# Optimization experiments

Measured on AMD Instinct MI355X. Metric: run time of the kernel, lower is better.

## Reference

```python
import jax, jax.numpy as jnp
import numpy as np

INPUTS = 512    # feature dim per timestep == seq len T == max_length (required by module math)
HIDDEN = 512
OUTPUTS = 512
MAXLEN = INPUTS
BATCH = 256


def setup_inputs() -> dict:
    key = jax.random.key(0)
    ks = jax.random.split(key, 7)
    def lin(k, out_f, in_f):
        bound = 1.0 / np.sqrt(in_f)
        return jax.random.uniform(k, (out_f, in_f), jnp.float32, -bound, bound)
    return {
        "x": jax.random.normal(ks[0], (BATCH, INPUTS * MAXLEN), jnp.float32),
        "W_attn": lin(ks[1], MAXLEN, HIDDEN + INPUTS),
        "b_attn": jnp.zeros((MAXLEN,), jnp.float32),
        "W_comb": lin(ks[2], HIDDEN, INPUTS + MAXLEN),
        "b_comb": jnp.zeros((HIDDEN,), jnp.float32),
        "W_ih": lin(ks[3], 3 * HIDDEN, HIDDEN),
        "W_hh": lin(ks[4], 3 * HIDDEN, HIDDEN),
        "b_ih": jnp.zeros((3 * HIDDEN,), jnp.float32),
        "b_hh": jnp.zeros((3 * HIDDEN,), jnp.float32),
        "W_out": lin(ks[5], OUTPUTS, HIDDEN),
        "b_out": jnp.zeros((OUTPUTS,), jnp.float32),
    }


def reference(x, W_attn, b_attn, W_comb, b_comb, W_ih, W_hh, b_ih, b_hh, W_out, b_out):
    B = x.shape[0]
    H = HIDDEN
    xv = x.reshape(B, INPUTS, MAXLEN)      # [B, inputs, T]
    xs = jnp.transpose(xv, (2, 0, 1))      # [T, B, inputs] for scan over time

    def step(h, x_t):
        # Bahdanau-style attention over the inputs axis (M == inputs)
        aw = jax.nn.softmax(jnp.concatenate([x_t, h], axis=1) @ W_attn.T + b_attn, axis=1)  # [B, M]
        ctx = jnp.einsum('bm,bmt->bt', aw, xv)                                              # [B, T]
        g = jax.nn.relu(jnp.concatenate([x_t, ctx], axis=1) @ W_comb.T + b_comb)            # [B, H]
        # PyTorch GRU cell, gate order (r, z, n)
        gi = g @ W_ih.T + b_ih
        gh = h @ W_hh.T + b_hh
        r = jax.nn.sigmoid(gi[:, :H] + gh[:, :H])
        z = jax.nn.sigmoid(gi[:, H:2 * H] + gh[:, H:2 * H])
        n = jnp.tanh(gi[:, 2 * H:] + r * gh[:, 2 * H:])
        h_new = (1.0 - z) * n + z * h
        return h_new, None

    h0 = jnp.zeros((B, H), x.dtype)
    hT, _ = jax.lax.scan(step, h0, xs)
    return hT @ W_out.T + b_out  # [B, outputs]
```

## Files before the change

### kernel.cpp

```cpp
#include <hip/hip_runtime.h>

#define NB 256
#define NT 512
#define NI 512
#define NH 512
#define NG 1536
#define NBLK 512

typedef __attribute__((ext_vector_type(8))) short bf16x8;
typedef __attribute__((ext_vector_type(4))) float f32x4;
typedef __attribute__((ext_vector_type(2))) float f32x2;

#define MFMA(a, b, c) __builtin_amdgcn_mfma_f32_16x16x32_bf16((a), (b), (c), 0, 0, 0)

#define BAR_LEAF(g)   ((g) * 64)
#define BAR_ROOT      1024
#define BAR_GEN       1088
#define FLG_LOGIT(rt) (1152 + (rt) * 64)
#define FLG_GH(rt)    (1664 + (rt) * 64)
#define FLG_XT        1920
#define FLG_G(rg)     (2176 + (rg) * 64)
#define FLG_GP(b)     (2688 + (b) * 64)
#define BAR_WORDS     20480

__device__ __forceinline__ unsigned short f2bf(float f) {
  unsigned int u = __float_as_uint(f);
  u = u + 0x7FFFu + ((u >> 16) & 1u);
  return (unsigned short)(u >> 16);
}
__device__ __forceinline__ float bflo(unsigned int p) { return __uint_as_float(p << 16); }
__device__ __forceinline__ float bfhi(unsigned int p) { return __uint_as_float(p & 0xffff0000u); }
__device__ __forceinline__ float sigm(float x) { return 1.f / (1.f + __expf(-x)); }

__device__ __forceinline__ void stf(float* p, float v) {
  __hip_atomic_store(p, v, __ATOMIC_RELAXED, __HIP_MEMORY_SCOPE_AGENT);
}
__device__ __forceinline__ void stu32(void* p, unsigned v) {
  __hip_atomic_store((unsigned*)p, v, __ATOMIC_RELAXED, __HIP_MEMORY_SCOPE_AGENT);
}
__device__ __forceinline__ void stu64(void* p, unsigned long long v) {
  __hip_atomic_store((unsigned long long*)p, v, __ATOMIC_RELAXED, __HIP_MEMORY_SCOPE_AGENT);
}
__device__ __forceinline__ void ldg16(uint4& d, const void* p) {
  asm volatile("global_load_dwordx4 %0, %1, off sc1" : "=v"(d) : "v"(p));
}
__device__ __forceinline__ void ldg8(float2& d, const void* p) {
  asm volatile("global_load_dwordx2 %0, %1, off sc1" : "=v"(d) : "v"(p));
}
__device__ __forceinline__ void ldg4(float& d, const void* p) {
  asm volatile("global_load_dword %0, %1, off sc1" : "=v"(d) : "v"(p));
}
__device__ __forceinline__ void wait_vm0() {
  asm volatile("s_waitcnt vmcnt(0)" ::: "memory");
  __builtin_amdgcn_sched_barrier(0);
}
__device__ __forceinline__ bf16x8 as_frag(uint4 v) {
  union { uint4 u; bf16x8 f; } c; c.u = v; return c.f;
}

__device__ __forceinline__ void flag_add(unsigned* f) {
  __hip_atomic_fetch_add(f, 1u, __ATOMIC_RELAXED, __HIP_MEMORY_SCOPE_AGENT);
}
__device__ __forceinline__ void flag_wait(unsigned* f, unsigned target) {
  while (__hip_atomic_load(f, __ATOMIC_RELAXED, __HIP_MEMORY_SCOPE_AGENT) < target)
    __builtin_amdgcn_s_sleep(1);
}

#define FP8_FMA16(PX, A_, ACC) do {                                              \
    f32x2 d0 = __builtin_amdgcn_cvt_pk_f32_fp8((int)(PX).x, false);              \
    f32x2 d1 = __builtin_amdgcn_cvt_pk_f32_fp8((int)(PX).x, true);               \
    f32x2 d2 = __builtin_amdgcn_cvt_pk_f32_fp8((int)(PX).y, false);              \
    f32x2 d3 = __builtin_amdgcn_cvt_pk_f32_fp8((int)(PX).y, true);               \
    f32x2 d4 = __builtin_amdgcn_cvt_pk_f32_fp8((int)(PX).z, false);              \
    f32x2 d5 = __builtin_amdgcn_cvt_pk_f32_fp8((int)(PX).z, true);               \
    f32x2 d6 = __builtin_amdgcn_cvt_pk_f32_fp8((int)(PX).w, false);              \
    f32x2 d7 = __builtin_amdgcn_cvt_pk_f32_fp8((int)(PX).w, true);               \
    (ACC)[0]  = fmaf((A_), d0[0], (ACC)[0]);  (ACC)[1]  = fmaf((A_), d0[1], (ACC)[1]);  \
    (ACC)[2]  = fmaf((A_), d1[0], (ACC)[2]);  (ACC)[3]  = fmaf((A_), d1[1], (ACC)[3]);  \
    (ACC)[4]  = fmaf((A_), d2[0], (ACC)[4]);  (ACC)[5]  = fmaf((A_), d2[1], (ACC)[5]);  \
    (ACC)[6]  = fmaf((A_), d3[0], (ACC)[6]);  (ACC)[7]  = fmaf((A_), d3[1], (ACC)[7]);  \
    (ACC)[8]  = fmaf((A_), d4[0], (ACC)[8]);  (ACC)[9]  = fmaf((A_), d4[1], (ACC)[9]);  \
    (ACC)[10] = fmaf((A_), d5[0], (ACC)[10]); (ACC)[11] = fmaf((A_), d5[1], (ACC)[11]); \
    (ACC)[12] = fmaf((A_), d6[0], (ACC)[12]); (ACC)[13] = fmaf((A_), d6[1], (ACC)[13]); \
    (ACC)[14] = fmaf((A_), d7[0], (ACC)[14]); (ACC)[15] = fmaf((A_), d7[1], (ACC)[15]); \
  } while (0)

__global__ __launch_bounds__(256) void cast_f32_bf16(const float* __restrict__ s,
                                                     unsigned short* __restrict__ d, int n) {
  int i = blockIdx.x * 256 + threadIdx.x;
  int stride = gridDim.x * 256;
  for (; i < n; i += stride) d[i] = f2bf(s[i]);
}

__global__ __launch_bounds__(256) void zt_fp8(unsigned short* __restrict__ XZ,
                                              float* __restrict__ Zsc,
                                              const unsigned short* __restrict__ Wc) {
  __shared__ unsigned short As[32][552];
  __shared__ float Zf[32][512];
  const int tid = threadIdx.x;
  const int row0 = blockIdx.x * 32;
  const uint4* src = (const uint4*)(XZ + (size_t)row0 * 512);
#pragma unroll
  for (int it = 0; it < 8; ++it) {
    int e8 = tid + it * 256;
    uint4 v = src[e8];
    *(uint4*)&As[e8 >> 6][(e8 & 63) * 8] = v;
  }
  __syncthreads();
  const int lane = tid & 63, w = tid >> 6;
  const int al = lane & 15, kg = lane >> 4;
  const int rbase = (w & 1) * 16;
  const int cbase = (w >> 1) * 256;
  for (int cc = 0; cc < 16; ++cc) {
    int col0 = cbase + cc * 16;
    f32x4 acc = {0.f, 0.f, 0.f, 0.f};
    const unsigned short* Bp = Wc + (size_t)(col0 + al) * 1024 + 512;
    for (int k = 0; k < 512; k += 32) {
      bf16x8 av = *(const bf16x8*)&As[rbase + al][k + kg * 8];
      bf16x8 bv = *(const bf16x8*)(Bp + k + kg * 8);
      acc = MFMA(av, bv, acc);
    }
#pragma unroll
    for (int r = 0; r < 4; ++r)
      Zf[rbase + kg * 4 + r][col0 + al] = acc[r];
  }
  __syncthreads();
  unsigned char* Z8 = (unsigned char*)XZ + ((size_t)blockIdx.x << 15);
#pragma unroll 2
  for (int r8 = 0; r8 < 8; ++r8) {
    int row = w * 8 + r8;
    const float* vr = &Zf[row][lane * 8];
    float v0 = vr[0], v1 = vr[1], v2 = vr[2], v3 = vr[3];
    float v4 = vr[4], v5 = vr[5], v6 = vr[6], v7 = vr[7];
    float amax = fmaxf(fmaxf(fmaxf(fabsf(v0), fabsf(v1)), fmaxf(fabsf(v2), fabsf(v3))),
                       fmaxf(fmaxf(fabsf(v4), fabsf(v5)), fmaxf(fabsf(v6), fabsf(v7))));
#pragma unroll
    for (int off = 32; off >= 1; off >>= 1) amax = fmaxf(amax, __shfl_xor(amax, off));
    float inv = amax > 0.f ? 448.f / amax : 0.f;
    int w0 = __builtin_amdgcn_cvt_pk_fp8_f32(v0 * inv, v1 * inv, 0, false);
    w0 = __builtin_amdgcn_cvt_pk_fp8_f32(v2 * inv, v3 * inv, w0, true);
    int w1 = __builtin_amdgcn_cvt_pk_fp8_f32(v4 * inv, v5 * inv, 0, false);
    w1 = __builtin_amdgcn_cvt_pk_fp8_f32(v6 * inv, v7 * inv, w1, true);
    uint2 o; o.x = (unsigned)w0; o.y = (unsigned)w1;
    *(uint2*)(Z8 + ((size_t)row << 9) + lane * 8) = o;
    if (lane == 0) Zsc[row0 + row] = amax * (1.f / 448.f);
  }
}

__global__ __launch_bounds__(256) void init_kernel(const float* __restrict__ x,
                                                   unsigned short* __restrict__ Xt,
                                                   unsigned short* __restrict__ Hbf,
                                                   unsigned* __restrict__ bar) {
  int idx = blockIdx.x * 256 + threadIdx.x;
  if (idx < BAR_WORDS) bar[idx] = 0u;
  if (idx < NB * NI) {
    int b = idx >> 9, i = idx & 511;
    Xt[idx] = f2bf(x[((size_t)b * 512 + i) * 512]);
    Hbf[idx] = 0;
  }
}

__global__ __launch_bounds__(256) void lxgx0_kernel(const unsigned short* __restrict__ Xt0,
                                                    const unsigned short* __restrict__ Wa,
                                                    const unsigned short* __restrict__ Wc,
                                                    const float* __restrict__ b_comb,
                                                    float* __restrict__ Lx,
                                                    float* __restrict__ Gx) {
  const int tid = threadIdx.x, lane = tid & 63, w = tid >> 6;
  const int al = lane & 15, kg = lane >> 4;
  int T = blockIdx.x;
  int m = T >> 7, tt = T & 127;
  int rt = tt >> 4, ct = tt & 15;
  int row0 = rt * 32 + (w & 1) * 16, col0 = ct * 32 + (w >> 1) * 16;
  const unsigned short* A = Xt0 + (size_t)(row0 + al) * NI;
  const unsigned short* B = (m ? Wc : Wa) + (size_t)(col0 + al) * 1024;
  f32x4 acc = {0.f, 0.f, 0.f, 0.f};
  for (int k = 0; k < 512; k += 32)
    acc = MFMA(*(const bf16x8*)(A + k + kg * 8), *(const bf16x8*)(B + k + kg * 8), acc);
  float* dst = m ? Gx : Lx;
  float bias = m ? b_comb[col0 + al] : 0.f;
#pragma unroll
  for (int r = 0; r < 4; ++r) {
    int row = row0 + kg * 4 + r;
    dst[row * NI + col0 + al] = acc[r] + bias;
  }
}

struct KParams {
  const unsigned char* Z8;
  const float* Zsc;
  const unsigned short* Wa;
  const unsigned short* Whh;
  const unsigned short* Wc;
  const unsigned short* Wih;
  const unsigned short* Wout;
  unsigned short* Xt;
  unsigned short* Hbf;
  unsigned short* Gbf;
  float* logits;
  float* gh;
  float* Lx;
  float* Gx;
  float* Gp;
  const float* x;
  const float* b_attn;
  const float* b_hh;
  const float* b_ih;
  const float* b_comb;
  const float* b_out;
  float* out;
  unsigned* bar;
};

__device__ __forceinline__ void gbar(unsigned* bar, unsigned gen_expect) {
  asm volatile("s_waitcnt vmcnt(0)" ::: "memory");
  __syncthreads();
  if (threadIdx.x == 0) {
    unsigned old = __hip_atomic_fetch_add(&bar[BAR_LEAF(blockIdx.x >> 5)], 1u,
                                          __ATOMIC_RELAXED, __HIP_MEMORY_SCOPE_AGENT);
    if ((old & 31) == 31) {
      unsigned ro = __hip_atomic_fetch_add(&bar[BAR_ROOT], 1u,
                                           __ATOMIC_RELAXED, __HIP_MEMORY_SCOPE_AGENT);
      if ((ro & 15) == 15)
        __hip_atomic_fetch_add(&bar[BAR_GEN], 1u,
                               __ATOMIC_RELAXED, __HIP_MEMORY_SCOPE_AGENT);
    }
    while (__hip_atomic_load(&bar[BAR_GEN], __ATOMIC_RELAXED, __HIP_MEMORY_SCOPE_AGENT) < gen_expect)
      __builtin_amdgcn_s_sleep(2);
    asm volatile("" ::: "memory");
  }
  __syncthreads();
}

__global__ __launch_bounds__(256, 2) void persistent_kernel(KParams P) {
  __shared__ __align__(16) unsigned char Zlds[65536];
  __shared__ float aw[512];
  __shared__ float pS[4][32][16];
  __shared__ float red[8];
  const int bid = blockIdx.x, tid = threadIdx.x;
  const int lane = tid & 63, w = tid >> 6;
  const int al = lane & 15, kg = lane >> 4;

  f32x4 hreg = {0.f, 0.f, 0.f, 0.f};

  const int b2_ = bid >> 1, mh_ = bid & 1;
  {
    const unsigned char* src = P.Z8 + ((size_t)(b2_ * 16 + mh_ * 8 + w * 2) << 15)
                               + (size_t)lane * 16;
    unsigned char* dst = &Zlds[w * 16384 + lane * 16];
#pragma unroll
    for (int k = 0; k < 16; ++k) {
      uint4 v = *(const uint4*)(src + ((size_t)k << 10));
      *(uint4*)(dst + (k << 10)) = v;
    }
  }

  for (int t = 0; t < NT; ++t) {
    const int p = t & 1, np = p ^ 1;
    if (bid < 128) {
      int rt = bid >> 4, ct = bid & 15;
      int row0 = rt * 32 + (w & 1) * 16, col0 = ct * 32 + (w >> 1) * 16;
      const unsigned short* Ah = P.Hbf + (size_t)(row0 + al) * NH;
      const unsigned short* B = P.Wa + (size_t)(col0 + al) * 1024 + 512;
      uint4 fh[16];
      float lx[4];
#pragma unroll
      for (int i = 0; i < 16; ++i) ldg16(fh[i], Ah + i * 32 + kg * 8);
      {
        const float* lxp = P.Lx + (size_t)p * (NB * NI) + (size_t)(row0 + kg * 4) * NI + col0 + al;
#pragma unroll
        for (int r = 0; r < 4; ++r) ldg4(lx[r], lxp + (size_t)r * NI);
      }
      wait_vm0();
      f32x4 a1 = {0.f, 0.f, 0.f, 0.f};
#pragma unroll
      for (int i = 0; i < 16; ++i)
        a1 = MFMA(as_frag(fh[i]), *(const bf16x8*)(B + i * 32 + kg * 8), a1);
#pragma unroll
      for (int r = 0; r < 4; ++r) {
        int row = row0 + kg * 4 + r;
        stf(&P.logits[row * NI + col0 + al], lx[r] + a1[r] + P.b_attn[col0 + al]);
      }
      __syncthreads();
      if (tid == 0) flag_add(&P.bar[FLG_LOGIT(rt)]);
    } else if (bid < 320) {
      int bb = bid - 128;
      int rt = bb / 48, ct = bb % 48;
      int row0 = rt * 64 + w * 16, col0 = ct * 32;
      const unsigned short* Ah = P.Hbf + (size_t)(row0 + al) * NH;
      const unsigned short* B0 = P.Whh + (size_t)(col0 + al) * 512;
      const unsigned short* B1 = P.Whh + (size_t)(col0 + 16 + al) * 512;
      uint4 fa[16];
#pragma unroll
      for (int i = 0; i < 16; ++i) ldg16(fa[i], Ah + i * 32 + kg * 8);
      wait_vm0();
      f32x4 a0 = {0.f, 0.f, 0.f, 0.f}, a1 = {0.f, 0.f, 0.f, 0.f};
#pragma unroll
      for (int i = 0; i < 16; ++i) {
        a0 = MFMA(as_frag(fa[i]), *(const bf16x8*)(B0 + i * 32 + kg * 8), a0);
        a1 = MFMA(as_frag(fa[i]), *(const bf16x8*)(B1 + i * 32 + kg * 8), a1);
      }
#pragma unroll
      for (int r = 0; r < 4; ++r) {
        int row = row0 + kg * 4 + r;
        stf(&P.gh[row * NG + col0 + al], a0[r] + P.b_hh[col0 + al]);
        stf(&P.gh[row * NG + col0 + 16 + al], a1[r] + P.b_hh[col0 + 16 + al]);
      }
      __syncthreads();
      if (tid == 0) flag_add(&P.bar[FLG_GH(rt)]);
    } else if (bid < 384) {
    } else {
      if (t < NT - 1) {
        for (int e2 = (bid - 384) * 256 + tid; e2 < NB * NI / 2; e2 += 128 * 256) {
          int b = e2 >> 8, i = (e2 & 255) * 2;
          const float* xp = P.x + ((size_t)b * 512 + i) * 512 + t + 1;
          unsigned lo = f2bf(xp[0]);
          unsigned hi = f2bf(xp[512]);
          stu32(&P.Xt[(size_t)np * (NB * NI) + b * 512 + i], lo | (hi << 16));
        }
        __syncthreads();
        if (tid == 0) flag_add(&P.bar[FLG_XT]);
      }
    }

    {
      const int b = b2_, mh = mh_;
      if (tid == 0) flag_wait(&P.bar[FLG_LOGIT(b >> 5)], 16u * (t + 1));
      __syncthreads();
      float2 lv;
      ldg8(lv, P.logits + (size_t)b * NI + 2 * tid);
      wait_vm0();
      float mx = fmaxf(lv.x, lv.y);
#pragma unroll
      for (int off = 32; off >= 1; off >>= 1) mx = fmaxf(mx, __shfl_xor(mx, off));
      if (lane == 0) red[w] = mx;
      __syncthreads();
      mx = fmaxf(fmaxf(red[0], red[1]), fmaxf(red[2], red[3]));
      float e0 = __expf(lv.x - mx), e1 = __expf(lv.y - mx);
      float sm = e0 + e1;
#pragma unroll
      for (int off = 32; off >= 1; off >>= 1) sm += __shfl_xor(sm, off);
      if (lane == 0) red[4 + w] = sm;
      __syncthreads();
      sm = (red[4] + red[5]) + (red[6] + red[7]);
      float inv = 1.f / sm;
      float2 scl = *(const float2*)(P.Zsc + (size_t)b * 512 + 2 * tid);
      aw[2 * tid] = e0 * inv * scl.x;
      aw[2 * tid + 1] = e1 * inv * scl.y;
      __syncthreads();

      const int half = lane >> 5, hl = lane & 31;
      const unsigned char* Zb1 = P.Z8 + ((size_t)(b * 16 + mh * 8 + w * 2 + 1) << 15)
                                + (size_t)lane * 16;
      const float* awp = aw + mh * 256 + w * 64;
      float acc[16];
#pragma unroll
      for (int i = 0; i < 16; ++i) acc[i] = 0.f;
      uint4 px[16];
#pragma unroll
      for (int k = 0; k < 16; ++k) px[k] = *(const uint4*)(Zb1 + ((size_t)k << 10));
      const unsigned char* Zl = &Zlds[w * 16384 + lane * 16];
#pragma unroll
      for (int k = 0; k < 16; ++k) {
        uint4 pl = *(const uint4*)(Zl + (k << 10));
        float a_ = awp[2 * k + half];
        FP8_FMA16(pl, a_, acc);
      }
#pragma unroll
      for (int k = 0; k < 16; ++k) {
        float a_ = awp[32 + 2 * k + half];
        FP8_FMA16(px[k], a_, acc);
      }
#pragma unroll
      for (int i = 0; i < 16; ++i) acc[i] += __shfl_xor(acc[i], 32);
      if (lane < 32) {
#pragma unroll
        for (int i = 0; i < 16; ++i) pS[w][hl][i] = acc[i];
      }
      __syncthreads();
      const int c0 = 2 * tid, c1 = 2 * tid + 1;
      float s0 = (pS[0][c0 >> 4][c0 & 15] + pS[1][c0 >> 4][c0 & 15])
               + (pS[2][c0 >> 4][c0 & 15] + pS[3][c0 >> 4][c0 & 15]);
      float s1 = (pS[0][c1 >> 4][c1 & 15] + pS[1][c1 >> 4][c1 & 15])
               + (pS[2][c1 >> 4][c1 & 15] + pS[3][c1 >> 4][c1 & 15]);
      if (mh == 0) {
        union { float f[2]; unsigned long long q; } q0;
        q0.f[0] = s0; q0.f[1] = s1;
        stu64(&P.Gp[(size_t)b * NH + c0], q0.q);
        __syncthreads();
        if (tid == 0) flag_add(&P.bar[FLG_GP(b)]);
      } else {
        __syncthreads();
        if (tid == 0) flag_wait(&P.bar[FLG_GP(b)], (unsigned)(t + 1));
        __syncthreads();
        float2 gp2, gx2;
        ldg8(gp2, &P.Gp[(size_t)b * NH + c0]);
        ldg8(gx2, P.Gx + (size_t)p * (NB * NH) + (size_t)b * NH + c0);
        wait_vm0();
        float v0 = fmaxf(gx2.x + gp2.x + s0, 0.f);
        float v1 = fmaxf(gx2.y + gp2.y + s1, 0.f);
        stu32(&P.Gbf[(size_t)b * NH + c0], (unsigned)f2bf(v0) | ((unsigned)f2bf(v1) << 16));
        __syncthreads();
        if (tid == 0) flag_add(&P.bar[FLG_G(b >> 5)]);
      }
    }

    if (bid >= 384) {
      int q = bid - 384;
      int rt = q >> 4, ct = q & 15;
      int row0 = rt * 32 + (w & 1) * 16;
      int j0 = ct * 32 + (w >> 1) * 16;
      if (tid == 0) {
        flag_wait(&P.bar[FLG_G(rt)], 32u * (t + 1));
        flag_wait(&P.bar[FLG_GH(rt >> 1)], 48u * (t + 1));
      }
      __syncthreads();
      const unsigned short* Ag = P.Gbf + (size_t)(row0 + al) * NH;
      const unsigned short* Br = P.Wih + (size_t)(j0 + al) * 512;
      const unsigned short* Bz = P.Wih + (size_t)(j0 + 512 + al) * 512;
      const unsigned short* Bn = P.Wih + (size_t)(j0 + 1024 + al) * 512;
      int j = j0 + al;
      uint4 fa[16];
      float ghv[4][3];
#pragma unroll
      for (int i = 0; i < 16; ++i) ldg16(fa[i], Ag + i * 32 + kg * 8);
#pragma unroll
      for (int r = 0; r < 4; ++r) {
        const float* ghrow = P.gh + (size_t)(row0 + kg * 4 + r) * NG + j;
        ldg4(ghv[r][0], ghrow);
        ldg4(ghv[r][1], ghrow + 512);
        ldg4(ghv[r][2], ghrow + 1024);
      }
      wait_vm0();
      f32x4 ar = {0.f, 0.f, 0.f, 0.f}, az = {0.f, 0.f, 0.f, 0.f}, an = {0.f, 0.f, 0.f, 0.f};
#pragma unroll
      for (int i = 0; i < 16; ++i) {
        ar = MFMA(as_frag(fa[i]), *(const bf16x8*)(Br + i * 32 + kg * 8), ar);
        az = MFMA(as_frag(fa[i]), *(const bf16x8*)(Bz + i * 32 + kg * 8), az);
        an = MFMA(as_frag(fa[i]), *(const bf16x8*)(Bn + i * 32 + kg * 8), an);
      }
      float bir = P.b_ih[j], biz = P.b_ih[j + 512], bin_ = P.b_ih[j + 1024];
#pragma unroll
      for (int r = 0; r < 4; ++r) {
        int row = row0 + kg * 4 + r;
        float rg = sigm(ar[r] + bir + ghv[r][0]);
        float zg = sigm(az[r] + biz + ghv[r][1]);
        float ng = tanhf(an[r] + bin_ + rg * ghv[r][2]);
        float hn = (1.f - zg) * ng + zg * hreg[r];
        hreg[r] = hn;
        unsigned hv = f2bf(hn);
        unsigned ov = __shfl_xor((int)hv, 1);
        if ((al & 1) == 0)
          stu32(&P.Hbf[(size_t)row * NH + (j & ~1)], hv | (ov << 16));
      }
    } else if (bid >= 320) {
      if (t < NT - 1) {
        if (tid == 0) flag_wait(&P.bar[FLG_XT], 128u * (t + 1));
        __syncthreads();
        int q = bid - 320;
        for (int jj = 0; jj < 4; ++jj) {
          int T = q + 64 * jj;
          int m = T >> 7, tt = T & 127;
          int rt = tt >> 4, ct = tt & 15;
          int row0 = rt * 32 + (w & 1) * 16, col0 = ct * 32 + (w >> 1) * 16;
          const unsigned short* A = P.Xt + (size_t)np * (NB * NI) + (size_t)(row0 + al) * NI;
          const unsigned short* B = (m ? P.Wc : P.Wa) + (size_t)(col0 + al) * 1024;
          uint4 fa[16];
#pragma unroll
          for (int i = 0; i < 16; ++i) ldg16(fa[i], A + i * 32 + kg * 8);
          wait_vm0();
          f32x4 acc = {0.f, 0.f, 0.f, 0.f};
#pragma unroll
          for (int i = 0; i < 16; ++i)
            acc = MFMA(as_frag(fa[i]), *(const bf16x8*)(B + i * 32 + kg * 8), acc);
          float* dst = (m ? P.Gx : P.Lx) + (size_t)np * (NB * NI);
          float bias = m ? P.b_comb[col0 + al] : 0.f;
#pragma unroll
          for (int r = 0; r < 4; ++r) {
            int row = row0 + kg * 4 + r;
            stf(&dst[row * NI + col0 + al], acc[r] + bias);
          }
        }
      }
    }
    gbar(P.bar, (unsigned)(t + 1));
  }

  if (bid < 128) {
    int rt = bid >> 4, ct = bid & 15;
    int row0 = rt * 32 + (w & 1) * 16;
    int col0 = ct * 32 + (w >> 1) * 16;
    const unsigned short* Ah = P.Hbf + (size_t)(row0 + al) * NH;
    const unsigned short* B0 = P.Wout + (size_t)(col0 + al) * 512;
    uint4 fa[16];
#pragma unroll
    for (int i = 0; i < 16; ++i) ldg16(fa[i], Ah + i * 32 + kg * 8);
    wait_vm0();
    f32x4 acc = {0.f, 0.f, 0.f, 0.f};
#pragma unroll
    for (int i = 0; i < 16; ++i) acc = MFMA(as_frag(fa[i]), *(const bf16x8*)(B0 + i * 32 + kg * 8), acc);
#pragma unroll
    for (int r = 0; r < 4; ++r) {
      int row = row0 + kg * 4 + r;
      P.out[row * 512 + col0 + al] = acc[r] + P.b_out[col0 + al];
    }
  }
}

extern "C" void kernel_launch(void* const* d_in, const int* in_sizes, int n_in,
                              void* d_out, int out_size, void* d_ws, size_t ws_size,
                              hipStream_t stream) {
  const float* x      = (const float*)d_in[0];
  const float* W_attn = (const float*)d_in[1];
  const float* b_attn = (const float*)d_in[2];
  const float* W_comb = (const float*)d_in[3];
  const float* b_comb = (const float*)d_in[4];
  const float* W_ih   = (const float*)d_in[5];
  const float* W_hh   = (const float*)d_in[6];
  const float* b_ih   = (const float*)d_in[7];
  const float* b_hh   = (const float*)d_in[8];
  const float* W_out  = (const float*)d_in[9];
  const float* b_out  = (const float*)d_in[10];

  char* wp = (char*)d_ws;
  size_t off = 0;
  unsigned short* XZ   = (unsigned short*)(wp + off); off += (size_t)NB * NI * NH * 2;
  unsigned short* Wa   = (unsigned short*)(wp + off); off += (size_t)NI * 1024 * 2;
  unsigned short* Whh  = (unsigned short*)(wp + off); off += (size_t)NG * 512 * 2;
  unsigned short* Wc   = (unsigned short*)(wp + off); off += (size_t)NH * 1024 * 2;
  unsigned short* Wih  = (unsigned short*)(wp + off); off += (size_t)NG * 512 * 2;
  unsigned short* Wout = (unsigned short*)(wp + off); off += (size_t)512 * 512 * 2;
  unsigned short* Xt   = (unsigned short*)(wp + off); off += (size_t)2 * NB * NI * 2;
  unsigned short* Hbf  = (unsigned short*)(wp + off); off += (size_t)NB * NH * 2;
  unsigned short* Gbf  = (unsigned short*)(wp + off); off += (size_t)NB * NH * 2;
  float* logits        = (float*)(wp + off); off += (size_t)NB * NI * 4;
  float* gh            = (float*)(wp + off); off += (size_t)NB * NG * 4;
  float* Lx            = (float*)(wp + off); off += (size_t)2 * NB * NI * 4;
  float* Gx            = (float*)(wp + off); off += (size_t)2 * NB * NI * 4;
  float* Gp            = (float*)(wp + off); off += (size_t)NB * NH * 4;
  float* Zsc           = (float*)(wp + off); off += (size_t)NB * NI * 4;
  unsigned* bar        = (unsigned*)(wp + off); off += (size_t)BAR_WORDS * 4 + 4096;

  cast_f32_bf16<<<8192, 256, 0, stream>>>(x, XZ, NB * NI * NT);
  cast_f32_bf16<<<512, 256, 0, stream>>>(W_attn, Wa, NI * 1024);
  cast_f32_bf16<<<512, 256, 0, stream>>>(W_hh, Whh, NG * 512);
  cast_f32_bf16<<<512, 256, 0, stream>>>(W_comb, Wc, NH * 1024);
  cast_f32_bf16<<<512, 256, 0, stream>>>(W_ih, Wih, NG * 512);
  cast_f32_bf16<<<512, 256, 0, stream>>>(W_out, Wout, 512 * 512);
  zt_fp8<<<4096, 256, 0, stream>>>(XZ, Zsc, Wc);
  init_kernel<<<512, 256, 0, stream>>>(x, Xt, Hbf, bar);
  lxgx0_kernel<<<256, 256, 0, stream>>>(Xt, Wa, Wc, b_comb, Lx, Gx);

  KParams prm;
  prm.Z8 = (const unsigned char*)XZ; prm.Zsc = Zsc;
  prm.Wa = Wa; prm.Whh = Whh; prm.Wc = Wc; prm.Wih = Wih; prm.Wout = Wout;
  prm.Xt = Xt; prm.Hbf = Hbf; prm.Gbf = Gbf;
  prm.logits = logits; prm.gh = gh; prm.Lx = Lx; prm.Gx = Gx; prm.Gp = Gp;
  prm.x = x; prm.b_attn = b_attn; prm.b_hh = b_hh; prm.b_ih = b_ih; prm.b_out = b_out;
  prm.b_comb = b_comb;
  prm.out = (float*)d_out;
  prm.bar = bar;

  void* kargs[] = { &prm };
  hipError_t e = hipLaunchCooperativeKernel((const void*)persistent_kernel,
                                            dim3(NBLK), dim3(256), kargs, 0, stream);
  if (e != hipSuccess) {
    persistent_kernel<<<dim3(NBLK), dim3(256), 0, stream>>>(prm);
  }
}
```

Measured before the change: 27.81 ms.

## Widen per-wave MFMA tiles to 64 columns and consolidate hidden-projection blocks

The logit and gh matmul roles now use 64-column tiles per wave with four accumulators, so each A fragment loaded from H is reused across four MFMAs. This cuts the logit blocks from 128 to 32 and the gh blocks from 192 to 96, with the flag-wait counts adjusted to match. The Xt projection role now covers one 32x128 tile per block instead of looping over four small tiles, which reloads the A fragments less often. The trade-off is more serial MFMA work per block on the recurrent critical path and more register pressure, while fewer blocks stay busy.

After: 36.36 ms. 1.31x slower.

```diff
diff --git a/kernel.cpp b/kernel.cpp
--- a/kernel.cpp
+++ b/kernel.cpp
@@ -28,8 +28,6 @@
   u = u + 0x7FFFu + ((u >> 16) & 1u);
   return (unsigned short)(u >> 16);
 }
-__device__ __forceinline__ float bflo(unsigned int p) { return __uint_as_float(p << 16); }
-__device__ __forceinline__ float bfhi(unsigned int p) { return __uint_as_float(p & 0xffff0000u); }
 __device__ __forceinline__ float sigm(float x) { return 1.f / (1.f + __expf(-x)); }
 
 __device__ __forceinline__ void stf(float* p, float v) {
@@ -257,55 +255,69 @@
 
   for (int t = 0; t < NT; ++t) {
     const int p = t & 1, np = p ^ 1;
-    if (bid < 128) {
-      int rt = bid >> 4, ct = bid & 15;
-      int row0 = rt * 32 + (w & 1) * 16, col0 = ct * 32 + (w >> 1) * 16;
+    if (bid < 32) {
+      int rt = bid >> 3, ct = bid & 7;
+      int row0 = rt * 64 + w * 16, col0 = ct * 64;
       const unsigned short* Ah = P.Hbf + (size_t)(row0 + al) * NH;
-      const unsigned short* B = P.Wa + (size_t)(col0 + al) * 1024 + 512;
       uint4 fh[16];
-      float lx[4];
+      float lx[4][4];
 #pragma unroll
       for (int i = 0; i < 16; ++i) ldg16(fh[i], Ah + i * 32 + kg * 8);
-      {
-        const float* lxp = P.Lx + (size_t)p * (NB * NI) + (size_t)(row0 + kg * 4) * NI + col0 + al;
-#pragma unroll
-        for (int r = 0; r < 4; ++r) ldg4(lx[r], lxp + (size_t)r * NI);
+#pragma unroll
+      for (int f = 0; f < 4; ++f) {
+        const float* lxp = P.Lx + (size_t)p * (NB * NI)
+                         + (size_t)(row0 + kg * 4) * NI + col0 + f * 16 + al;
+#pragma unroll
+        for (int r = 0; r < 4; ++r) ldg4(lx[f][r], lxp + (size_t)r * NI);
       }
       wait_vm0();
-      f32x4 a1 = {0.f, 0.f, 0.f, 0.f};
-#pragma unroll
-      for (int i = 0; i < 16; ++i)
-        a1 = MFMA(as_frag(fh[i]), *(const bf16x8*)(B + i * 32 + kg * 8), a1);
-#pragma unroll
-      for (int r = 0; r < 4; ++r) {
-        int row = row0 + kg * 4 + r;
-        stf(&P.logits[row * NI + col0 + al], lx[r] + a1[r] + P.b_attn[col0 + al]);
-      }
+      f32x4 a[4] = {{0,0,0,0},{0,0,0,0},{0,0,0,0},{0,0,0,0}};
+#pragma unroll
+      for (int i = 0; i < 16; ++i) {
+        bf16x8 av = as_frag(fh[i]);
+#pragma unroll
+        for (int f = 0; f < 4; ++f) {
+          const unsigned short* B = P.Wa + (size_t)(col0 + f * 16 + al) * 1024 + 512;
+          a[f] = MFMA(av, *(const bf16x8*)(B + i * 32 + kg * 8), a[f]);
+        }
+      }
+#pragma unroll
+      for (int f = 0; f < 4; ++f)
+#pragma unroll
+        for (int r = 0; r < 4; ++r) {
+          int row = row0 + kg * 4 + r;
+          stf(&P.logits[row * NI + col0 + f * 16 + al],
+              lx[f][r] + a[f][r] + P.b_attn[col0 + f * 16 + al]);
+        }
       __syncthreads();
       if (tid == 0) flag_add(&P.bar[FLG_LOGIT(rt)]);
-    } else if (bid < 320) {
-      int bb = bid - 128;
-      int rt = bb / 48, ct = bb % 48;
-      int row0 = rt * 64 + w * 16, col0 = ct * 32;
+    } else if (bid < 128) {
+      int bb = bid - 32;
+      int rt = bb / 24, ct = bb % 24;
+      int row0 = rt * 64 + w * 16, col0 = ct * 64;
       const unsigned short* Ah = P.Hbf + (size_t)(row0 + al) * NH;
-      const unsigned short* B0 = P.Whh + (size_t)(col0 + al) * 512;
-      const unsigned short* B1 = P.Whh + (size_t)(col0 + 16 + al) * 512;
       uint4 fa[16];
 #pragma unroll
       for (int i = 0; i < 16; ++i) ldg16(fa[i], Ah + i * 32 + kg * 8);
       wait_vm0();
-      f32x4 a0 = {0.f, 0.f, 0.f, 0.f}, a1 = {0.f, 0.f, 0.f, 0.f};
+      f32x4 a[4] = {{0,0,0,0},{0,0,0,0},{0,0,0,0},{0,0,0,0}};
 #pragma unroll
       for (int i = 0; i < 16; ++i) {
-        a0 = MFMA(as_frag(fa[i]), *(const bf16x8*)(B0 + i * 32 + kg * 8), a0);
-        a1 = MFMA(as_frag(fa[i]), *(const bf16x8*)(B1 + i * 32 + kg * 8), a1);
-      }
-#pragma unroll
-      for (int r = 0; r < 4; ++r) {
-        int row = row0 + kg * 4 + r;
-        stf(&P.gh[row * NG + col0 + al], a0[r] + P.b_hh[col0 + al]);
-        stf(&P.gh[row * NG + col0 + 16 + al], a1[r] + P.b_hh[col0 + 16 + al]);
-      }
+        bf16x8 av = as_frag(fa[i]);
+#pragma unroll
+        for (int f = 0; f < 4; ++f) {
+          const unsigned short* B = P.Whh + (size_t)(col0 + f * 16 + al) * 512;
+          a[f] = MFMA(av, *(const bf16x8*)(B + i * 32 + kg * 8), a[f]);
+        }
+      }
+#pragma unroll
+      for (int f = 0; f < 4; ++f)
+#pragma unroll
+        for (int r = 0; r < 4; ++r) {
+          int row = row0 + kg * 4 + r;
+          stf(&P.gh[row * NG + col0 + f * 16 + al],
+              a[f][r] + P.b_hh[col0 + f * 16 + al]);
+        }
       __syncthreads();
       if (tid == 0) flag_add(&P.bar[FLG_GH(rt)]);
     } else if (bid < 384) {
@@ -325,7 +337,7 @@
 
     {
       const int b = b2_, mh = mh_;
-      if (tid == 0) flag_wait(&P.bar[FLG_LOGIT(b >> 5)], 16u * (t + 1));
+      if (tid == 0) flag_wait(&P.bar[FLG_LOGIT(b >> 6)], 8u * (t + 1));
       __syncthreads();
       float2 lv;
       ldg8(lv, P.logits + (size_t)b * NI + 2 * tid);
@@ -412,7 +424,7 @@
       int j0 = ct * 32 + (w >> 1) * 16;
       if (tid == 0) {
         flag_wait(&P.bar[FLG_G(rt)], 32u * (t + 1));
-        flag_wait(&P.bar[FLG_GH(rt >> 1)], 48u * (t + 1));
+        flag_wait(&P.bar[FLG_GH(rt >> 1)], 24u * (t + 1));
       }
       __syncthreads();
       const unsigned short* Ag = P.Gbf + (size_t)(row0 + al) * NH;
@@ -458,27 +470,36 @@
         if (tid == 0) flag_wait(&P.bar[FLG_XT], 128u * (t + 1));
         __syncthreads();
         int q = bid - 320;
-        for (int jj = 0; jj < 4; ++jj) {
-          int T = q + 64 * jj;
-          int m = T >> 7, tt = T & 127;
-          int rt = tt >> 4, ct = tt & 15;
-          int row0 = rt * 32 + (w & 1) * 16, col0 = ct * 32 + (w >> 1) * 16;
-          const unsigned short* A = P.Xt + (size_t)np * (NB * NI) + (size_t)(row0 + al) * NI;
-          const unsigned short* B = (m ? P.Wc : P.Wa) + (size_t)(col0 + al) * 1024;
-          uint4 fa[16];
-#pragma unroll
-          for (int i = 0; i < 16; ++i) ldg16(fa[i], A + i * 32 + kg * 8);
-          wait_vm0();
-          f32x4 acc = {0.f, 0.f, 0.f, 0.f};
-#pragma unroll
-          for (int i = 0; i < 16; ++i)
-            acc = MFMA(as_frag(fa[i]), *(const bf16x8*)(B + i * 32 + kg * 8), acc);
-          float* dst = (m ? P.Gx : P.Lx) + (size_t)np * (NB * NI);
-          float bias = m ? P.b_comb[col0 + al] : 0.f;
+        int rg = q >> 3, ctl = q & 7;
+        int wr = w & 1, wc = w >> 1;
+        int row0 = rg * 32 + wr * 16;
+        int colb = ctl * 128 + wc * 64;
+        const unsigned short* A = P.Xt + (size_t)np * (NB * NI) + (size_t)(row0 + al) * NI;
+        uint4 fa[16];
+#pragma unroll
+        for (int i = 0; i < 16; ++i) ldg16(fa[i], A + i * 32 + kg * 8);
+        wait_vm0();
+        int m = (colb >= 512);
+        int cb = colb - (m ? 512 : 0);
+        const unsigned short* Wb = m ? P.Wc : P.Wa;
+        f32x4 a[4] = {{0,0,0,0},{0,0,0,0},{0,0,0,0},{0,0,0,0}};
+#pragma unroll
+        for (int i = 0; i < 16; ++i) {
+          bf16x8 av = as_frag(fa[i]);
+#pragma unroll
+          for (int f = 0; f < 4; ++f) {
+            const unsigned short* B = Wb + (size_t)(cb + f * 16 + al) * 1024;
+            a[f] = MFMA(av, *(const bf16x8*)(B + i * 32 + kg * 8), a[f]);
+          }
+        }
+        float* dst = (m ? P.Gx : P.Lx) + (size_t)np * (NB * NI);
+#pragma unroll
+        for (int f = 0; f < 4; ++f) {
+          float bias = m ? P.b_comb[cb + f * 16 + al] : 0.f;
 #pragma unroll
           for (int r = 0; r < 4; ++r) {
             int row = row0 + kg * 4 + r;
-            stf(&dst[row * NI + col0 + al], acc[r] + bias);
+            stf(&dst[row * NI + cb + f * 16 + al], a[f][r] + bias);
           }
         }
       }
```
